# Optimization experiments

Measured on AMD Instinct MI355X. Metric: run time of the kernel, lower is better.

## Reference

```python
import jax, jax.numpy as jnp
import numpy as np

R, MAXI, MAXO = 333, 119, 12   # n ROIs, max roi input size, max roi reduced size
E, H = 3328, 8                  # embed dim (concat 3325 + pad 3), heads
HD = E // H                     # 416
CONCAT = 3325
EPS = 1e-5


def _roi_layout():
    """Deterministic synthetic ROI sizes + gather maps for vectorized ragged encode."""
    sizes = 30 + (7 * np.arange(R)) % 90            # per-ROI input widths
    reduced = 8 + np.arange(R) % 5                  # per-ROI output widths
    reduced[332] = 8                                # makes concat+3 divisible by 8
    starts = np.concatenate([[0], np.cumsum(sizes)[:-1]])
    total = int(sizes.sum())                        # 24696
    in_idx = np.minimum(starts[:, None] + np.arange(MAXI)[None, :], total - 1)
    in_mask = (np.arange(MAXI)[None, :] < sizes[:, None]).astype(np.float32)
    out_idx = np.concatenate([i * MAXO + np.arange(reduced[i]) for i in range(R)])
    assert out_idx.shape[0] == CONCAT
    return jnp.asarray(in_idx), jnp.asarray(in_mask), jnp.asarray(out_idx)


def _bn(x, g, b):
    # training-mode BatchNorm1d: biased batch stats (matches torch normalization)
    m = x.mean(0)
    v = x.var(0)
    return (x - m) * jax.lax.rsqrt(v + EPS) * g + b


def _lrelu(x, s):
    return jnp.where(x > 0, x, s * x)


def setup_inputs() -> dict:
    key = jax.random.key(0)
    ks = jax.random.split(key, 16)
    B, TOTAL = 2048, 24696
    f32 = jnp.float32
    return {
        'x': jax.random.normal(ks[0], (B, TOTAL), f32),
        'enc_W': jax.random.normal(ks[1], (R, MAXO, MAXI), f32) * 0.1,
        'enc_b': jax.random.normal(ks[2], (R, MAXO), f32) * 0.02,
        'bn1_g': jnp.ones((CONCAT,), f32),
        'bn1_b': jnp.zeros((CONCAT,), f32),
        'Wqkv': jax.random.normal(ks[3], (3 * E, E), f32) * (1.0 / np.sqrt(E)),
        'bqkv': jnp.zeros((3 * E,), f32),
        'Wo': jax.random.normal(ks[4], (E, E), f32) * (1.0 / np.sqrt(E)),
        'bo': jnp.zeros((E,), f32),
        'W1': jax.random.normal(ks[5], (1024, E), f32) * (1.0 / np.sqrt(E)),
        'b1': jnp.zeros((1024,), f32),
        'bn2_g': jnp.ones((1024,), f32),
        'bn2_b': jnp.zeros((1024,), f32),
        'W2': jax.random.normal(ks[6], (300, 1024), f32) * (1.0 / 32.0),
        'b2': jnp.zeros((300,), f32),
        'Wc': jax.random.normal(ks[7], (180, 300), f32) * 0.06,
        'bc': jnp.zeros((180,), f32),
    }


def reference(x, enc_W, enc_b, bn1_g, bn1_b, Wqkv, bqkv, Wo, bo,
              W1, b1, bn2_g, bn2_b, W2, b2, Wc, bc):
    in_idx, in_mask, out_idx = _roi_layout()
    B = x.shape[0]
    # --- vectorized ragged per-ROI Linear (replaces 333-way python loop) ---
    xp = x[:, in_idx] * in_mask                     # [B, R, MAXI], padded slices
    y = jnp.einsum('bri,roi->bro', xp, enc_W) + enc_b  # [B, R, MAXO]
    y = y.reshape(B, R * MAXO)[:, out_idx]          # ragged concat -> [B, 3325]
    # per-ROI BN+LeakyReLU(0.3) == per-feature on the concat
    y = _lrelu(_bn(y, bn1_g, bn1_b), 0.3)
    y = jnp.pad(y, ((0, 0), (1, 2)))                # F.pad (1, 2) -> [B, 3328]
    # --- MultiheadAttention, seq_len = 1 (input unsqueezed to [1, B, E]) ---
    qkv = y @ Wqkv.T + bqkv                         # [B, 3E]
    q, k, v = jnp.split(qkv, 3, axis=-1)
    q = q.reshape(B, H, 1, HD)
    k = k.reshape(B, H, 1, HD)
    v = v.reshape(B, H, 1, HD)
    s = jnp.einsum('bhqd,bhkd->bhqk', q, k) / jnp.sqrt(jnp.float32(HD))
    a = jax.nn.softmax(s, axis=-1)                  # trivially 1 for L=1, kept faithful
    o = jnp.einsum('bhqk,bhkd->bhqd', a, v).reshape(B, E)
    o = o @ Wo.T + bo
    r = _lrelu(_bn(o @ W1.T + b1, bn2_g, bn2_b), 0.1)
    reg_out = r @ W2.T + b2                         # [B, 300]
    y_pred = jax.nn.softmax(reg_out @ Wc.T + bc, axis=-1)  # [B, 180]
    return reg_out, y_pred
```

## Files before the change

### kernel.cpp

```cpp
#include <hip/hip_runtime.h>
#include <hip/hip_bf16.h>

#define B_      2048
#define R_      333
#define MAXI_   119
#define MAXO_   12
#define CONCAT_ 3325
#define E_      3328
#define TOTAL_  24696
#define HID_    1024
#define NREG_   300
#define NCLS_   180
#define EPS_    1e-5f
#define NS2_    128

typedef __attribute__((ext_vector_type(8))) short bf16x8;
typedef __attribute__((ext_vector_type(4))) float f32x4;

static __device__ inline unsigned short f2bf_rne(float f) {
  unsigned u;
  __builtin_memcpy(&u, &f, 4);
  u += 0x7fff + ((u >> 16) & 1);
  return (unsigned short)(u >> 16);
}
static __device__ inline float bf2f(unsigned short s) {
  unsigned u = (unsigned)s << 16;
  float f;
  __builtin_memcpy(&f, &u, 4);
  return f;
}

__global__ void layout_kernel(int* __restrict__ starts, int* __restrict__ red_starts) {
  if (threadIdx.x == 0 && blockIdx.x == 0) {
    int s = 0, rs = 0;
    for (int r = 0; r < R_; ++r) {
      starts[r] = s;
      red_starts[r] = rs;
      s += 30 + (7 * r) % 90;
      rs += (r == 332) ? 8 : (8 + r % 5);
    }
  }
}

__device__ __forceinline__ void rowdot_body(
    const float* __restrict__ A, const float* __restrict__ v, const float* __restrict__ b,
    float* __restrict__ out, int N, int K, int jb) {
  int wid = threadIdx.x >> 6, lane = threadIdx.x & 63;
  int j = jb * 4 + wid;
  if (j >= N) return;
  const float* row = A + (size_t)j * K;
  float s = 0.f;
  for (int k = lane; k < K; k += 64) s = fmaf(row[k], v[k], s);
  for (int o = 32; o; o >>= 1) s += __shfl_down(s, o);
  if (lane == 0) out[j] = s + b[j];
}

__device__ __forceinline__ void pack_w_body(const float* __restrict__ enc_W,
                                            const int* __restrict__ starts,
                                            unsigned short* __restrict__ Wpk, int r) {
  int tid = threadIdx.x;
  int kc = tid >> 6, lane = tid & 63;
  int size = 30 + (7 * r) % 90;
  int s8 = starts[r] & 7;
  int oc = lane & 15;
  int k0 = kc * 32 + (lane >> 4) * 8;
  unsigned short o[8];
#pragma unroll
  for (int e = 0; e < 8; ++e) {
    int k = k0 + e - s8;
    float v = 0.f;
    if (oc < MAXO_ && k >= 0 && k < size) v = enc_W[((size_t)r * MAXO_ + oc) * MAXI_ + k];
    o[e] = f2bf_rne(v);
  }
  unsigned short* dst = Wpk + ((size_t)r * 4 + kc) * 512 + lane * 8;
  *(ushort4*)dst = *(ushort4*)&o[0];
  *(ushort4*)(dst + 4) = *(ushort4*)&o[4];
}

#define NTR_    ((E_ / 64) * (E_ / 64))
#define NC4A_   (HID_ * E_ / 4)
#define NC4B_   (NREG_ * HID_ / 4)
#define NCAST_  ((NC4A_ + NC4B_ + 255) / 256)
__global__ __launch_bounds__(256) void prep_kernel(
    const float* __restrict__ Wo, const float* __restrict__ Wv,
    unsigned short* __restrict__ WoT, unsigned short* __restrict__ WvT,
    const float* __restrict__ W1, unsigned short* __restrict__ W1b,
    const float* __restrict__ W2, unsigned short* __restrict__ W2b,
    const float* __restrict__ bv, const float* __restrict__ bo, float* __restrict__ t1v,
    const float* __restrict__ enc_W, const int* __restrict__ starts,
    unsigned short* __restrict__ Wpk) {
  __shared__ float tile[64][65];
  int bid = blockIdx.x;
  if (bid < 2 * NTR_) {
    int z = bid / NTR_, rem = bid % NTR_;
    const float* in = z ? Wv : Wo;
    unsigned short* out = z ? WvT : WoT;
    int c0 = (rem % 52) * 64, r0 = (rem / 52) * 64;
    int t = threadIdx.x;
    int ci = t & 63, ri0 = t >> 6;
    for (int ri = ri0; ri < 64; ri += 4)
      tile[ri][ci] = in[(size_t)(r0 + ri) * E_ + c0 + ci];
    __syncthreads();
    int rj = t & 63, i0 = t >> 6;
    for (int i = i0; i < 64; i += 4)
      out[(size_t)(c0 + i) * E_ + r0 + rj] = f2bf_rne(tile[rj][i]);
  } else if (bid < 2 * NTR_ + NCAST_) {
    int i = (bid - 2 * NTR_) * 256 + threadIdx.x;
    const float* src; unsigned short* dst; int idx;
    if (i < NC4A_) { src = W1; dst = W1b; idx = i; }
    else if (i < NC4A_ + NC4B_) { src = W2; dst = W2b; idx = i - NC4A_; }
    else return;
    float4 v = ((const float4*)src)[idx];
    ushort4 o;
    o.x = f2bf_rne(v.x); o.y = f2bf_rne(v.y); o.z = f2bf_rne(v.z); o.w = f2bf_rne(v.w);
    ((ushort4*)dst)[idx] = o;
  } else if (bid < 2 * NTR_ + NCAST_ + E_ / 4) {
    rowdot_body(Wo, bv, bo, t1v, E_, E_, bid - 2 * NTR_ - NCAST_);
  } else {
    pack_w_body(enc_W, starts, Wpk, bid - 2 * NTR_ - NCAST_ - E_ / 4);
  }
}

__device__ __forceinline__ void encode_body(
    const float* __restrict__ x, const unsigned short* __restrict__ Wpk,
    const float* __restrict__ enc_b, const int* __restrict__ starts,
    const int* __restrict__ red_starts,
    unsigned short* __restrict__ yT, int r, int bg) {
  int tid = threadIdx.x;
  int wid = tid >> 6, lane = tid & 63;
  int lr = lane & 15, kg = lane >> 4;

  int size = 30 + (7 * r) % 90;
  int red  = (r == 332) ? 8 : (8 + r % 5);
  int st   = starts[r];
  int s8   = st & 7;
  int a0   = st & ~7;
  int rs   = red_starts[r];
  int nkc  = (s8 + size + 31) >> 5;
  int kmax = TOTAL_ - a0;

  bf16x8 wf[4];
  const unsigned short* wp = Wpk + (size_t)r * 2048 + lane * 8;
#pragma unroll
  for (int kc = 0; kc < 4; ++kc) wf[kc] = *(const bf16x8*)(wp + kc * 512);

  float bofs[4];
#pragma unroll
  for (int reg = 0; reg < 4; ++reg) {
    int oc = kg * 4 + reg;
    bofs[reg] = (oc < MAXO_) ? enc_b[r * MAXO_ + oc] : 0.f;
  }

  int b0 = bg * 64 + wid * 16;
  const float* xrow = x + (size_t)(b0 + lr) * TOTAL_ + a0;
  f32x4 acc = {0.f, 0.f, 0.f, 0.f};
#pragma unroll
  for (int kc = 0; kc < 4; ++kc) {
    if (kc < nkc) {
      int k0 = kc * 32 + kg * 8;
      if (k0 + 8 > kmax) k0 = kmax - 8;
      float4 v0 = *(const float4*)(xrow + k0);
      float4 v1 = *(const float4*)(xrow + k0 + 4);
      bf16x8 xf;
      xf[0] = (short)f2bf_rne(v0.x); xf[1] = (short)f2bf_rne(v0.y);
      xf[2] = (short)f2bf_rne(v0.z); xf[3] = (short)f2bf_rne(v0.w);
      xf[4] = (short)f2bf_rne(v1.x); xf[5] = (short)f2bf_rne(v1.y);
      xf[6] = (short)f2bf_rne(v1.z); xf[7] = (short)f2bf_rne(v1.w);
      acc = __builtin_amdgcn_mfma_f32_16x16x32_bf16(wf[kc], xf, acc, 0, 0, 0);
    }
  }
#pragma unroll
  for (int reg = 0; reg < 4; ++reg) {
    int oc = kg * 4 + reg;
    if (oc < red)
      yT[(size_t)(rs + oc) * B_ + b0 + lr] = f2bf_rne(acc[reg] + bofs[reg]);
  }
}

template <int KS, bool OUT_BF16>
__device__ __forceinline__ void gemm_body(
    const unsigned short* __restrict__ A, const unsigned short* __restrict__ W,
    float* __restrict__ Cf, unsigned short* __restrict__ Cb,
    int M, int N, int K, int bx, int by, int bz, unsigned short* smem) {
  unsigned short* a_lds = smem;
  unsigned short* b_lds = smem + 8192;
  int tid = threadIdx.x;
  int wid = tid >> 6, lane = tid & 63;
  int wr = wid >> 1, wc = wid & 1;
  int row0 = by * 128, col0 = bx * 128;
  int lr = lane & 15, kg = lane >> 4;
  int Klocal = K / KS;
  int kbase = bz * Klocal;

  int srow = tid >> 2, sk = (tid & 3) * 8;
  const unsigned short* aptr0 = A + (size_t)(row0 + srow) * K + kbase + sk;
  const unsigned short* aptr1 = aptr0 + (size_t)64 * K;
  int bcol0 = col0 + srow;      if (bcol0 > N - 1) bcol0 = N - 1;
  int bcol1 = col0 + 64 + srow; if (bcol1 > N - 1) bcol1 = N - 1;
  const unsigned short* bptr0 = W + (size_t)bcol0 * K + kbase + sk;
  const unsigned short* bptr1 = W + (size_t)bcol1 * K + kbase + sk;

  f32x4 acc[4][4] = {};
  int nk = Klocal >> 5;

#define STAGE_(buf, kc)                                                                             \
  do {                                                                                              \
    __builtin_amdgcn_global_load_lds((const __attribute__((address_space(1))) void*)(aptr0 + (kc)), \
        (__attribute__((address_space(3))) void*)(a_lds + (buf) * 4096 + wid * 512), 16, 0, 0);     \
    __builtin_amdgcn_global_load_lds((const __attribute__((address_space(1))) void*)(aptr1 + (kc)), \
        (__attribute__((address_space(3))) void*)(a_lds + (buf) * 4096 + 2048 + wid * 512), 16, 0, 0); \
    __builtin_amdgcn_global_load_lds((const __attribute__((address_space(1))) void*)(bptr0 + (kc)), \
        (__attribute__((address_space(3))) void*)(b_lds + (buf) * 4096 + wid * 512), 16, 0, 0);     \
    __builtin_amdgcn_global_load_lds((const __attribute__((address_space(1))) void*)(bptr1 + (kc)), \
        (__attribute__((address_space(3))) void*)(b_lds + (buf) * 4096 + 2048 + wid * 512), 16, 0, 0); \
  } while (0)

  STAGE_(0, 0);
  __syncthreads();
  int cur = 0;
  for (int t = 0; t < nk; ++t) {
    if (t + 1 < nk) STAGE_(cur ^ 1, (t + 1) * 32);
    bf16x8 a[4], b[4];
#pragma unroll
    for (int f = 0; f < 4; ++f) {
      a[f] = *(const bf16x8*)(a_lds + cur * 4096 + (wr * 64 + f * 16 + lr) * 32 + kg * 8);
      b[f] = *(const bf16x8*)(b_lds + cur * 4096 + (wc * 64 + f * 16 + lr) * 32 + kg * 8);
    }
#pragma unroll
    for (int i = 0; i < 4; ++i)
#pragma unroll
      for (int j = 0; j < 4; ++j)
        acc[i][j] = __builtin_amdgcn_mfma_f32_16x16x32_bf16(a[i], b[j], acc[i][j], 0, 0, 0);
    __syncthreads();
    cur ^= 1;
  }
#undef STAGE_

#pragma unroll
  for (int j = 0; j < 4; ++j) {
    int ccol = col0 + wc * 64 + j * 16 + lr;
    if (ccol >= N) continue;
#pragma unroll
    for (int i = 0; i < 4; ++i) {
#pragma unroll
      for (int reg = 0; reg < 4; ++reg) {
        int crow = row0 + wr * 64 + i * 16 + kg * 4 + reg;
        float v = acc[i][j][reg];
        if (KS == 1) {
          if (OUT_BF16) Cb[(size_t)crow * N + ccol] = f2bf_rne(v);
          else          Cf[(size_t)crow * N + ccol] = v;
        } else {
          Cf[((size_t)bz * M + crow) * N + ccol] = v;
        }
      }
    }
  }
}

#define WA_NB_   ((E_ / 128) * (HID_ / 128))
#define ENCH_NB_ (R_ * 16)
__global__ __launch_bounds__(256) void mega_a_kernel(
    const float* __restrict__ x, const unsigned short* __restrict__ Wpk,
    const float* __restrict__ enc_b, const int* __restrict__ starts,
    const int* __restrict__ red_starts, unsigned short* __restrict__ yT,
    const unsigned short* __restrict__ W1b, const unsigned short* __restrict__ WoT,
    unsigned short* __restrict__ Wa_bf,
    const float* __restrict__ W1, const float* __restrict__ t1v,
    const float* __restrict__ b1, float* __restrict__ zbv) {
  __shared__ __align__(16) unsigned short smem[16384];
  int bid = blockIdx.x;
  if (bid < WA_NB_) {
    gemm_body<1, true>(W1b, WoT, nullptr, Wa_bf, HID_, E_, E_,
                       bid % (E_ / 128), bid / (E_ / 128), 0, smem);
  } else if (bid < WA_NB_ + ENCH_NB_) {
    int eb = bid - WA_NB_;
    encode_body(x, Wpk, enc_b, starts, red_starts, yT, eb >> 4, eb & 15);
  } else {
    rowdot_body(W1, t1v, b1, zbv, HID_, E_, bid - WA_NB_ - ENCH_NB_);
  }
}

#define WB2_NB_ (WA_NB_ * 2)
__global__ __launch_bounds__(256) void mega_b_kernel(
    const float* __restrict__ x, const unsigned short* __restrict__ Wpk,
    const float* __restrict__ enc_b, const int* __restrict__ starts,
    const int* __restrict__ red_starts, unsigned short* __restrict__ yT,
    const unsigned short* __restrict__ Wa_bf, const unsigned short* __restrict__ WvT,
    float* __restrict__ Cpart) {
  __shared__ __align__(16) unsigned short smem[16384];
  int bid = blockIdx.x;
  if (bid < WB2_NB_) {
    int z = bid / WA_NB_, rem = bid % WA_NB_;
    gemm_body<2, false>(Wa_bf, WvT, Cpart, nullptr, HID_, E_, E_,
                        rem % (E_ / 128), rem / (E_ / 128), z, smem);
  } else {
    int eb = bid - WB2_NB_;
    encode_body(x, Wpk, enc_b, starts, red_starts, yT, eb >> 4, 16 + (eb & 15));
  }
}

#define ST_NB_  ((CONCAT_ + 15) / 16)
#define CWB_NB_ (HID_ * E_ / 4 / 256)
__global__ __launch_bounds__(256) void stats_comb_kernel(
    const unsigned short* __restrict__ yT, float* __restrict__ mean, float* __restrict__ rstd,
    const float* __restrict__ Cpart, unsigned short* __restrict__ Wb_bf) {
  int bid = blockIdx.x;
  if (bid < ST_NB_) {
    int t = threadIdx.x;
    int f = bid * 16 + (t >> 4);
    int j = t & 15;
    if (f >= CONCAT_) return;
    const unsigned short* p = yT + (size_t)f * B_ + j * 128;
    float s = 0.f, s2 = 0.f;
#pragma unroll
    for (int i = 0; i < 16; ++i) {
      bf16x8 v = *(const bf16x8*)(p + i * 8);
#pragma unroll
      for (int e = 0; e < 8; ++e) {
        float xv = bf2f((unsigned short)v[e]);
        s += xv; s2 = fmaf(xv, xv, s2);
      }
    }
#pragma unroll
    for (int m = 1; m <= 8; m <<= 1) { s += __shfl_xor(s, m); s2 += __shfl_xor(s2, m); }
    if (j == 0) {
      float mm = s / B_;
      float var = s2 / B_ - mm * mm;
      mean[f] = mm;
      rstd[f] = rsqrtf(var + EPS_);
    }
  } else {
    int i4 = (bid - ST_NB_) * 256 + threadIdx.x;
    const int MN4 = HID_ * E_ / 4;
    if (i4 >= MN4) return;
    float4 a = ((const float4*)Cpart)[i4];
    float4 b = ((const float4*)(Cpart + (size_t)HID_ * E_))[i4];
    ushort4 o;
    o.x = f2bf_rne(a.x + b.x); o.y = f2bf_rne(a.y + b.y);
    o.z = f2bf_rne(a.z + b.z); o.w = f2bf_rne(a.w + b.w);
    ((ushort4*)Wb_bf)[i4] = o;
  }
}

#define TR_NB_ ((E_ / 64) * (B_ / 64))
__global__ __launch_bounds__(256) void bn1_transpose_kernel(
    const unsigned short* __restrict__ yT, const float* __restrict__ mean,
    const float* __restrict__ rstd, const float* __restrict__ g,
    const float* __restrict__ bb, unsigned short* __restrict__ Y) {
  __shared__ float tile[64][65];
  int bid = blockIdx.x;
  int cc0 = (bid % 52) * 64, b0 = (bid / 52) * 64;
  int t = threadIdx.x;
  int bi = t & 63, ci0 = t >> 6;
  for (int ci = ci0; ci < 64; ci += 4) {
    int c = cc0 + ci - 1;
    float v = 0.f;
    if (c >= 0 && c < CONCAT_) {
      float f = bf2f(yT[(size_t)c * B_ + b0 + bi]);
      v = (f - mean[c]) * rstd[c] * g[c] + bb[c];
      v = v > 0.f ? v : 0.3f * v;
    }
    tile[ci][bi] = v;
  }
  __syncthreads();
  int cj = t & 63, bj0 = t >> 6;
  for (int bj = bj0; bj < 64; bj += 4)
    Y[(size_t)(b0 + bj) * E_ + cc0 + cj] = f2bf_rne(tile[cj][bj]);
}

template <int KS, bool OUT_BF16>
__global__ __launch_bounds__(256) void gemm_kernel(
    const unsigned short* __restrict__ A, const unsigned short* __restrict__ W,
    float* __restrict__ Cf, unsigned short* __restrict__ Cb, int M, int N, int K) {
  __shared__ __align__(16) unsigned short smem[16384];
  gemm_body<KS, OUT_BF16>(A, W, Cf, Cb, M, N, K, blockIdx.x, blockIdx.y, blockIdx.z, smem);
}

__global__ __launch_bounds__(256) void combZ_stats_kernel(
    const float* __restrict__ Cpart, const float* __restrict__ zb,
    float* __restrict__ Z, float* __restrict__ pS, float* __restrict__ pS2) {
  int c = blockIdx.x * 256 + threadIdx.x;
  int ry = blockIdx.y;
  float zbc = zb[c];
  float s1 = 0.f, s2 = 0.f;
  for (int r = ry * 16; r < ry * 16 + 16; ++r) {
    float v = zbc;
#pragma unroll
    for (int z = 0; z < 4; ++z) v += Cpart[((size_t)z * B_ + r) * HID_ + c];
    Z[(size_t)r * HID_ + c] = v;
    s1 += v; s2 = fmaf(v, v, s2);
  }
  pS[ry * HID_ + c] = s1;
  pS2[ry * HID_ + c] = s2;
}

__global__ __launch_bounds__(256) void colstats_final_kernel(
    const float* __restrict__ pS, const float* __restrict__ pS2,
    float* __restrict__ mean, float* __restrict__ rstd) {
  int c = blockIdx.x * 256 + threadIdx.x;
  if (c >= HID_) return;
  float s = 0.f, s2 = 0.f;
  for (int i = 0; i < NS2_; ++i) { s += pS[i * HID_ + c]; s2 += pS2[i * HID_ + c]; }
  float m = s / B_;
  float v = s2 / B_ - m * m;
  mean[c] = m;
  rstd[c] = rsqrtf(v + EPS_);
}

__global__ __launch_bounds__(256) void bn2_apply_kernel(
    const float* __restrict__ Z, const float* __restrict__ mean, const float* __restrict__ rstd,
    const float* __restrict__ g, const float* __restrict__ bb, unsigned short* __restrict__ R) {
  int i = blockIdx.x * 256 + threadIdx.x;
  int c = i & (HID_ - 1);
  float v = (Z[i] - mean[c]) * rstd[c] * g[c] + bb[c];
  v = v > 0.f ? v : 0.1f * v;
  R[i] = f2bf_rne(v);
}

__global__ __launch_bounds__(256) void classifier_kernel(
    const float* __restrict__ Cpart, const float* __restrict__ b2,
    const float* __restrict__ Wc, const float* __restrict__ bc,
    float* __restrict__ reg_out, float* __restrict__ ypred) {
  int b = blockIdx.x;
  __shared__ __align__(16) float rrow[NREG_];
  __shared__ float sl[256];
  int tid = threadIdx.x;
  for (int i = tid; i < NREG_; i += 256) {
    float s = b2[i];
#pragma unroll
    for (int z = 0; z < 4; ++z) s += Cpart[((size_t)z * B_ + b) * NREG_ + i];
    rrow[i] = s;
    reg_out[(size_t)b * NREG_ + i] = s;
  }
  __syncthreads();
  float s = -1e30f;
  if (tid < NCLS_) {
    const float* w = Wc + (size_t)tid * NREG_;
    float acc = 0.f;
    for (int k = 0; k < NREG_; k += 4) {
      float4 wv = *(const float4*)(w + k);
      float4 rv = *(const float4*)(&rrow[k]);
      acc = fmaf(wv.x, rv.x, acc); acc = fmaf(wv.y, rv.y, acc);
      acc = fmaf(wv.z, rv.z, acc); acc = fmaf(wv.w, rv.w, acc);
    }
    s = acc + bc[tid];
  }
  sl[tid] = s;
  __syncthreads();
  for (int o = 128; o > 0; o >>= 1) {
    if (tid < o) sl[tid] = fmaxf(sl[tid], sl[tid + o]);
    __syncthreads();
  }
  float mx = sl[0];
  __syncthreads();
  float e = (tid < NCLS_) ? __expf(s - mx) : 0.f;
  sl[tid] = e;
  __syncthreads();
  for (int o = 128; o > 0; o >>= 1) {
    if (tid < o) sl[tid] += sl[tid + o];
    __syncthreads();
  }
  if (tid < NCLS_) ypred[(size_t)b * NCLS_ + tid] = e / sl[0];
}

extern "C" void kernel_launch(void* const* d_in, const int* in_sizes, int n_in,
                              void* d_out, int out_size, void* d_ws, size_t ws_size,
                              hipStream_t stream) {
  const float* x     = (const float*)d_in[0];
  const float* enc_W = (const float*)d_in[1];
  const float* enc_b = (const float*)d_in[2];
  const float* bn1_g = (const float*)d_in[3];
  const float* bn1_b = (const float*)d_in[4];
  const float* Wqkv  = (const float*)d_in[5];
  const float* bqkv  = (const float*)d_in[6];
  const float* Wo    = (const float*)d_in[7];
  const float* bo    = (const float*)d_in[8];
  const float* W1    = (const float*)d_in[9];
  const float* b1    = (const float*)d_in[10];
  const float* bn2_g = (const float*)d_in[11];
  const float* bn2_b = (const float*)d_in[12];
  const float* W2    = (const float*)d_in[13];
  const float* b2    = (const float*)d_in[14];
  const float* Wc    = (const float*)d_in[15];
  const float* bc    = (const float*)d_in[16];

  char* ws = (char*)d_ws;
  size_t off = 0;
  auto alloc = [&](size_t bytes) -> void* {
    void* p = ws + off;
    off += (bytes + 255) & ~(size_t)255;
    return p;
  };

  unsigned short* yT     = (unsigned short*)alloc((size_t)CONCAT_ * B_ * 2);
  float*          mean1  = (float*)alloc(CONCAT_ * 4);
  float*          rstd1  = (float*)alloc(CONCAT_ * 4);
  unsigned short* Ybf    = (unsigned short*)alloc((size_t)B_ * E_ * 2);
  unsigned short* Rbf    = (unsigned short*)alloc((size_t)B_ * HID_ * 2);
  unsigned short* WoT_bf = (unsigned short*)alloc((size_t)E_ * E_ * 2);
  unsigned short* WvT_bf = (unsigned short*)alloc((size_t)E_ * E_ * 2);
  unsigned short* W1_bf  = (unsigned short*)alloc((size_t)HID_ * E_ * 2);
  unsigned short* W2_bf  = (unsigned short*)alloc((size_t)NREG_ * HID_ * 2);
  unsigned short* Wa_bf  = (unsigned short*)alloc((size_t)HID_ * E_ * 2);
  unsigned short* Wb_bf  = (unsigned short*)alloc((size_t)HID_ * E_ * 2);
  unsigned short* Wpk    = (unsigned short*)alloc((size_t)R_ * 2048 * 2);
  float*          Cpart  = (float*)alloc((size_t)4 * B_ * HID_ * 4);
  float*          t1v    = (float*)alloc(E_ * 4);
  float*          zbv    = (float*)alloc(HID_ * 4);
  float*          partS  = (float*)alloc((size_t)NS2_ * HID_ * 4);
  float*          partS2 = (float*)alloc((size_t)NS2_ * HID_ * 4);
  float*          mean2  = (float*)alloc(HID_ * 4);
  float*          rstd2  = (float*)alloc(HID_ * 4);
  int*            starts = (int*)alloc(R_ * 4);
  int*            redst  = (int*)alloc(R_ * 4);

  float* Z = (float*)yT;

  layout_kernel<<<1, 1, 0, stream>>>(starts, redst);
  prep_kernel<<<2 * NTR_ + NCAST_ + E_ / 4 + R_, 256, 0, stream>>>(
      Wo, Wqkv + (size_t)2 * E_ * E_, WoT_bf, WvT_bf,
      W1, W1_bf, W2, W2_bf, bqkv + 2 * E_, bo, t1v, enc_W, starts, Wpk);
  mega_a_kernel<<<WA_NB_ + ENCH_NB_ + HID_ / 4, 256, 0, stream>>>(
      x, Wpk, enc_b, starts, redst, yT, W1_bf, WoT_bf, Wa_bf, W1, t1v, b1, zbv);
  mega_b_kernel<<<WB2_NB_ + ENCH_NB_, 256, 0, stream>>>(
      x, Wpk, enc_b, starts, redst, yT, Wa_bf, WvT_bf, Cpart);
  stats_comb_kernel<<<ST_NB_ + CWB_NB_, 256, 0, stream>>>(
      yT, mean1, rstd1, Cpart, Wb_bf);
  bn1_transpose_kernel<<<TR_NB_, 256, 0, stream>>>(
      yT, mean1, rstd1, bn1_g, bn1_b, Ybf);
  gemm_kernel<4, false><<<dim3(HID_ / 128, B_ / 128, 4), 256, 0, stream>>>(
      Ybf, Wb_bf, Cpart, nullptr, B_, HID_, E_);
  combZ_stats_kernel<<<dim3(HID_ / 256, NS2_), 256, 0, stream>>>(Cpart, zbv, Z, partS, partS2);
  colstats_final_kernel<<<(HID_ + 255) / 256, 256, 0, stream>>>(partS, partS2, mean2, rstd2);
  bn2_apply_kernel<<<(B_ * HID_) / 256, 256, 0, stream>>>(Z, mean2, rstd2, bn2_g, bn2_b, Rbf);
  gemm_kernel<4, false><<<dim3((NREG_ + 127) / 128, B_ / 128, 4), 256, 0, stream>>>(
      Rbf, W2_bf, Cpart, nullptr, B_, NREG_, HID_);
  float* reg_out = (float*)d_out;
  classifier_kernel<<<B_, 256, 0, stream>>>(
      Cpart, b2, Wc, bc, reg_out, reg_out + (size_t)B_ * NREG_);
}
```

Baseline: 312.7 us.

## Stage x chunks in LDS for ROI encode; drop split-K in weight-fold GEMM

Result: slower. 360.3 us (+15.2%).

```diff
diff --git a/kernel.cpp b/kernel.cpp
--- a/kernel.cpp
+++ b/kernel.cpp
@@ -13,6 +13,9 @@
 #define NCLS_   180
 #define EPS_    1e-5f
 #define NS2_    128
+#define CHN_    49
+#define CHW_    640
+#define XSTR_   648
 
 typedef __attribute__((ext_vector_type(8))) short bf16x8;
 typedef __attribute__((ext_vector_type(4))) float f32x4;
@@ -30,12 +33,17 @@
   return f;
 }
 
-__global__ void layout_kernel(int* __restrict__ starts, int* __restrict__ red_starts) {
+__global__ void layout_kernel(int* __restrict__ starts, int* __restrict__ red_starts,
+                              int* __restrict__ chunk_first, int* __restrict__ chunk_cnt) {
   if (threadIdx.x == 0 && blockIdx.x == 0) {
+    for (int c = 0; c < CHN_; ++c) { chunk_first[c] = 0; chunk_cnt[c] = 0; }
     int s = 0, rs = 0;
     for (int r = 0; r < R_; ++r) {
       starts[r] = s;
       red_starts[r] = rs;
+      int c = s >> 9;
+      if (chunk_cnt[c] == 0) chunk_first[c] = r;
+      chunk_cnt[c]++;
       s += 30 + (7 * r) % 90;
       rs += (r == 332) ? 8 : (8 + r % 5);
     }
@@ -121,59 +129,58 @@
   }
 }
 
-__device__ __forceinline__ void encode_body(
+__device__ __forceinline__ void encode64_body(
     const float* __restrict__ x, const unsigned short* __restrict__ Wpk,
     const float* __restrict__ enc_b, const int* __restrict__ starts,
-    const int* __restrict__ red_starts,
-    unsigned short* __restrict__ yT, int r, int bg) {
+    const int* __restrict__ red_starts, const int* __restrict__ chunk_first,
+    const int* __restrict__ chunk_cnt, unsigned short* __restrict__ yT,
+    unsigned short* __restrict__ xt , int c, int bt) {
   int tid = threadIdx.x;
   int wid = tid >> 6, lane = tid & 63;
+  int base = c << 9;
+  int row0 = bt * 16;
+
+  for (int rr = wid * 4; rr < wid * 4 + 4; ++rr) {
+    const float* src = x + (size_t)(row0 + rr) * TOTAL_ + base;
+#pragma unroll
+    for (int j = 0; j < 3; ++j) {
+      int col = j * 256 + lane * 4;
+      if (col < CHW_) {
+        float4 v = {0.f, 0.f, 0.f, 0.f};
+        if (base + col < TOTAL_) v = *(const float4*)(src + col);
+        ushort4 o;
+        o.x = f2bf_rne(v.x); o.y = f2bf_rne(v.y); o.z = f2bf_rne(v.z); o.w = f2bf_rne(v.w);
+        *(ushort4*)&xt[rr * XSTR_ + col] = o;
+      }
+    }
+  }
+  __syncthreads();
+
   int lr = lane & 15, kg = lane >> 4;
-
-  int size = 30 + (7 * r) % 90;
-  int red  = (r == 332) ? 8 : (8 + r % 5);
-  int st   = starts[r];
-  int s8   = st & 7;
-  int a0   = st & ~7;
-  int rs   = red_starts[r];
-  int nkc  = (s8 + size + 31) >> 5;
-  int kmax = TOTAL_ - a0;
-
-  bf16x8 wf[4];
-  const unsigned short* wp = Wpk + (size_t)r * 2048 + lane * 8;
-#pragma unroll
-  for (int kc = 0; kc < 4; ++kc) wf[kc] = *(const bf16x8*)(wp + kc * 512);
-
-  float bofs[4];
-#pragma unroll
-  for (int reg = 0; reg < 4; ++reg) {
-    int oc = kg * 4 + reg;
-    bofs[reg] = (oc < MAXO_) ? enc_b[r * MAXO_ + oc] : 0.f;
-  }
-
-  int b0 = bg * 64 + wid * 16;
-  const float* xrow = x + (size_t)(b0 + lr) * TOTAL_ + a0;
-  f32x4 acc = {0.f, 0.f, 0.f, 0.f};
-#pragma unroll
-  for (int kc = 0; kc < 4; ++kc) {
-    if (kc < nkc) {
-      int k0 = kc * 32 + kg * 8;
-      if (k0 + 8 > kmax) k0 = kmax - 8;
-      float4 v0 = *(const float4*)(xrow + k0);
-      float4 v1 = *(const float4*)(xrow + k0 + 4);
-      bf16x8 xf;
-      xf[0] = (short)f2bf_rne(v0.x); xf[1] = (short)f2bf_rne(v0.y);
-      xf[2] = (short)f2bf_rne(v0.z); xf[3] = (short)f2bf_rne(v0.w);
-      xf[4] = (short)f2bf_rne(v1.x); xf[5] = (short)f2bf_rne(v1.y);
-      xf[6] = (short)f2bf_rne(v1.z); xf[7] = (short)f2bf_rne(v1.w);
-      acc = __builtin_amdgcn_mfma_f32_16x16x32_bf16(wf[kc], xf, acc, 0, 0, 0);
-    }
-  }
-#pragma unroll
-  for (int reg = 0; reg < 4; ++reg) {
-    int oc = kg * 4 + reg;
-    if (oc < red)
-      yT[(size_t)(rs + oc) * B_ + b0 + lr] = f2bf_rne(acc[reg] + bofs[reg]);
+  int first = chunk_first[c], cnt = chunk_cnt[c];
+  for (int ri = wid; ri < cnt; ri += 4) {
+    int r = first + ri;
+    int size = 30 + (7 * r) % 90;
+    int red  = (r == 332) ? 8 : (8 + r % 5);
+    int st   = starts[r];
+    int s8   = st & 7;
+    int ls8  = (st - base) & ~7;
+    int rs   = red_starts[r];
+    int nkc  = (s8 + size + 31) >> 5;
+
+    f32x4 acc = {0.f, 0.f, 0.f, 0.f};
+    const unsigned short* wp = Wpk + (size_t)r * 2048 + lane * 8;
+    for (int kc = 0; kc < nkc; ++kc) {
+      bf16x8 wf = *(const bf16x8*)(wp + kc * 512);
+      bf16x8 xf = *(const bf16x8*)&xt[lr * XSTR_ + ls8 + kc * 32 + kg * 8];
+      acc = __builtin_amdgcn_mfma_f32_16x16x32_bf16(wf, xf, acc, 0, 0, 0);
+    }
+#pragma unroll
+    for (int reg = 0; reg < 4; ++reg) {
+      int oc = kg * 4 + reg;
+      if (oc < red)
+        yT[(size_t)(rs + oc) * B_ + row0 + lr] = f2bf_rne(acc[reg] + enc_b[r * MAXO_ + oc]);
+    }
   }
 }
 
@@ -258,11 +265,12 @@
 }
 
 #define WA_NB_   ((E_ / 128) * (HID_ / 128))
-#define ENCH_NB_ (R_ * 16)
+#define ENCH_NB_ (CHN_ * 64)
 __global__ __launch_bounds__(256) void mega_a_kernel(
     const float* __restrict__ x, const unsigned short* __restrict__ Wpk,
     const float* __restrict__ enc_b, const int* __restrict__ starts,
-    const int* __restrict__ red_starts, unsigned short* __restrict__ yT,
+    const int* __restrict__ red_starts, const int* __restrict__ chF,
+    const int* __restrict__ chC, unsigned short* __restrict__ yT,
     const unsigned short* __restrict__ W1b, const unsigned short* __restrict__ WoT,
     unsigned short* __restrict__ Wa_bf,
     const float* __restrict__ W1, const float* __restrict__ t1v,
@@ -274,71 +282,57 @@
                        bid % (E_ / 128), bid / (E_ / 128), 0, smem);
   } else if (bid < WA_NB_ + ENCH_NB_) {
     int eb = bid - WA_NB_;
-    encode_body(x, Wpk, enc_b, starts, red_starts, yT, eb >> 4, eb & 15);
+    encode64_body(x, Wpk, enc_b, starts, red_starts, chF, chC, yT, smem,
+                  eb / 64, eb % 64);
   } else {
     rowdot_body(W1, t1v, b1, zbv, HID_, E_, bid - WA_NB_ - ENCH_NB_);
   }
 }
 
-#define WB2_NB_ (WA_NB_ * 2)
 __global__ __launch_bounds__(256) void mega_b_kernel(
     const float* __restrict__ x, const unsigned short* __restrict__ Wpk,
     const float* __restrict__ enc_b, const int* __restrict__ starts,
-    const int* __restrict__ red_starts, unsigned short* __restrict__ yT,
+    const int* __restrict__ red_starts, const int* __restrict__ chF,
+    const int* __restrict__ chC, unsigned short* __restrict__ yT,
     const unsigned short* __restrict__ Wa_bf, const unsigned short* __restrict__ WvT,
-    float* __restrict__ Cpart) {
+    unsigned short* __restrict__ Wb_bf) {
   __shared__ __align__(16) unsigned short smem[16384];
   int bid = blockIdx.x;
-  if (bid < WB2_NB_) {
-    int z = bid / WA_NB_, rem = bid % WA_NB_;
-    gemm_body<2, false>(Wa_bf, WvT, Cpart, nullptr, HID_, E_, E_,
-                        rem % (E_ / 128), rem / (E_ / 128), z, smem);
+  if (bid < WA_NB_) {
+    gemm_body<1, true>(Wa_bf, WvT, nullptr, Wb_bf, HID_, E_, E_,
+                       bid % (E_ / 128), bid / (E_ / 128), 0, smem);
   } else {
-    int eb = bid - WB2_NB_;
-    encode_body(x, Wpk, enc_b, starts, red_starts, yT, eb >> 4, 16 + (eb & 15));
+    int eb = bid - WA_NB_;
+    encode64_body(x, Wpk, enc_b, starts, red_starts, chF, chC, yT, smem,
+                  eb / 64, 64 + eb % 64);
   }
 }
 
 #define ST_NB_  ((CONCAT_ + 15) / 16)
-#define CWB_NB_ (HID_ * E_ / 4 / 256)
-__global__ __launch_bounds__(256) void stats_comb_kernel(
-    const unsigned short* __restrict__ yT, float* __restrict__ mean, float* __restrict__ rstd,
-    const float* __restrict__ Cpart, unsigned short* __restrict__ Wb_bf) {
-  int bid = blockIdx.x;
-  if (bid < ST_NB_) {
-    int t = threadIdx.x;
-    int f = bid * 16 + (t >> 4);
-    int j = t & 15;
-    if (f >= CONCAT_) return;
-    const unsigned short* p = yT + (size_t)f * B_ + j * 128;
-    float s = 0.f, s2 = 0.f;
-#pragma unroll
-    for (int i = 0; i < 16; ++i) {
-      bf16x8 v = *(const bf16x8*)(p + i * 8);
-#pragma unroll
-      for (int e = 0; e < 8; ++e) {
-        float xv = bf2f((unsigned short)v[e]);
-        s += xv; s2 = fmaf(xv, xv, s2);
-      }
-    }
-#pragma unroll
-    for (int m = 1; m <= 8; m <<= 1) { s += __shfl_xor(s, m); s2 += __shfl_xor(s2, m); }
-    if (j == 0) {
-      float mm = s / B_;
-      float var = s2 / B_ - mm * mm;
-      mean[f] = mm;
-      rstd[f] = rsqrtf(var + EPS_);
-    }
-  } else {
-    int i4 = (bid - ST_NB_) * 256 + threadIdx.x;
-    const int MN4 = HID_ * E_ / 4;
-    if (i4 >= MN4) return;
-    float4 a = ((const float4*)Cpart)[i4];
-    float4 b = ((const float4*)(Cpart + (size_t)HID_ * E_))[i4];
-    ushort4 o;
-    o.x = f2bf_rne(a.x + b.x); o.y = f2bf_rne(a.y + b.y);
-    o.z = f2bf_rne(a.z + b.z); o.w = f2bf_rne(a.w + b.w);
-    ((ushort4*)Wb_bf)[i4] = o;
+__global__ __launch_bounds__(256) void bn1_stats_kernel(
+    const unsigned short* __restrict__ yT, float* __restrict__ mean, float* __restrict__ rstd) {
+  int t = threadIdx.x;
+  int f = blockIdx.x * 16 + (t >> 4);
+  int j = t & 15;
+  if (f >= CONCAT_) return;
+  const unsigned short* p = yT + (size_t)f * B_ + j * 128;
+  float s = 0.f, s2 = 0.f;
+#pragma unroll
+  for (int i = 0; i < 16; ++i) {
+    bf16x8 v = *(const bf16x8*)(p + i * 8);
+#pragma unroll
+    for (int e = 0; e < 8; ++e) {
+      float xv = bf2f((unsigned short)v[e]);
+      s += xv; s2 = fmaf(xv, xv, s2);
+    }
+  }
+#pragma unroll
+  for (int m = 1; m <= 8; m <<= 1) { s += __shfl_xor(s, m); s2 += __shfl_xor(s2, m); }
+  if (j == 0) {
+    float mm = s / B_;
+    float var = s2 / B_ - mm * mm;
+    mean[f] = mm;
+    rstd[f] = rsqrtf(var + EPS_);
   }
 }
 
@@ -513,19 +507,20 @@
   float*          rstd2  = (float*)alloc(HID_ * 4);
   int*            starts = (int*)alloc(R_ * 4);
   int*            redst  = (int*)alloc(R_ * 4);
+  int*            chF    = (int*)alloc(CHN_ * 4);
+  int*            chC    = (int*)alloc(CHN_ * 4);
 
   float* Z = (float*)yT;
 
-  layout_kernel<<<1, 1, 0, stream>>>(starts, redst);
+  layout_kernel<<<1, 1, 0, stream>>>(starts, redst, chF, chC);
   prep_kernel<<<2 * NTR_ + NCAST_ + E_ / 4 + R_, 256, 0, stream>>>(
       Wo, Wqkv + (size_t)2 * E_ * E_, WoT_bf, WvT_bf,
       W1, W1_bf, W2, W2_bf, bqkv + 2 * E_, bo, t1v, enc_W, starts, Wpk);
   mega_a_kernel<<<WA_NB_ + ENCH_NB_ + HID_ / 4, 256, 0, stream>>>(
-      x, Wpk, enc_b, starts, redst, yT, W1_bf, WoT_bf, Wa_bf, W1, t1v, b1, zbv);
-  mega_b_kernel<<<WB2_NB_ + ENCH_NB_, 256, 0, stream>>>(
-      x, Wpk, enc_b, starts, redst, yT, Wa_bf, WvT_bf, Cpart);
-  stats_comb_kernel<<<ST_NB_ + CWB_NB_, 256, 0, stream>>>(
-      yT, mean1, rstd1, Cpart, Wb_bf);
+      x, Wpk, enc_b, starts, redst, chF, chC, yT, W1_bf, WoT_bf, Wa_bf, W1, t1v, b1, zbv);
+  mega_b_kernel<<<WA_NB_ + ENCH_NB_, 256, 0, stream>>>(
+      x, Wpk, enc_b, starts, redst, chF, chC, yT, Wa_bf, WvT_bf, Wb_bf);
+  bn1_stats_kernel<<<ST_NB_, 256, 0, stream>>>(yT, mean1, rstd1);
   bn1_transpose_kernel<<<TR_NB_, 256, 0, stream>>>(
       yT, mean1, rstd1, bn1_g, bn1_b, Ybf);
   gemm_kernel<4, false><<<dim3(HID_ / 128, B_ / 128, 4), 256, 0, stream>>>(
```

## Rebalance prep work across mega kernels and split BN1 stats into halves

Applied to the files above, without the earlier changes.

Measured after the change: 330.6 us. 1.06x slower.

```diff
diff --git a/kernel.cpp b/kernel.cpp
--- a/kernel.cpp
+++ b/kernel.cpp
@@ -77,47 +77,40 @@
   *(ushort4*)(dst + 4) = *(ushort4*)&o[4];
 }
 
-#define NTR_    ((E_ / 64) * (E_ / 64))
-#define NC4A_   (HID_ * E_ / 4)
-#define NC4B_   (NREG_ * HID_ / 4)
-#define NCAST_  ((NC4A_ + NC4B_ + 255) / 256)
+__device__ __forceinline__ void transpose_body(
+    const float* __restrict__ in, unsigned short* __restrict__ out,
+    int tileIdx, void* smem) {
+  float (*tile)[65] = (float(*)[65])smem;
+  int c0 = (tileIdx % 52) * 64, r0 = (tileIdx / 52) * 64;
+  int t = threadIdx.x;
+  int ci = t & 63, ri0 = t >> 6;
+  for (int ri = ri0; ri < 64; ri += 4)
+    tile[ri][ci] = in[(size_t)(r0 + ri) * E_ + c0 + ci];
+  __syncthreads();
+  int rj = t & 63, i0 = t >> 6;
+  for (int i = i0; i < 64; i += 4)
+    out[(size_t)(c0 + i) * E_ + r0 + rj] = f2bf_rne(tile[rj][i]);
+}
+
+#define NTR_     ((E_ / 64) * (E_ / 64))
+#define W1C_NB_  (HID_ * E_ / 4 / 256)
 __global__ __launch_bounds__(256) void prep_kernel(
-    const float* __restrict__ Wo, const float* __restrict__ Wv,
-    unsigned short* __restrict__ WoT, unsigned short* __restrict__ WvT,
+    const float* __restrict__ Wo, unsigned short* __restrict__ WoT,
     const float* __restrict__ W1, unsigned short* __restrict__ W1b,
-    const float* __restrict__ W2, unsigned short* __restrict__ W2b,
-    const float* __restrict__ bv, const float* __restrict__ bo, float* __restrict__ t1v,
     const float* __restrict__ enc_W, const int* __restrict__ starts,
     unsigned short* __restrict__ Wpk) {
   __shared__ float tile[64][65];
   int bid = blockIdx.x;
-  if (bid < 2 * NTR_) {
-    int z = bid / NTR_, rem = bid % NTR_;
-    const float* in = z ? Wv : Wo;
-    unsigned short* out = z ? WvT : WoT;
-    int c0 = (rem % 52) * 64, r0 = (rem / 52) * 64;
-    int t = threadIdx.x;
-    int ci = t & 63, ri0 = t >> 6;
-    for (int ri = ri0; ri < 64; ri += 4)
-      tile[ri][ci] = in[(size_t)(r0 + ri) * E_ + c0 + ci];
-    __syncthreads();
-    int rj = t & 63, i0 = t >> 6;
-    for (int i = i0; i < 64; i += 4)
-      out[(size_t)(c0 + i) * E_ + r0 + rj] = f2bf_rne(tile[rj][i]);
-  } else if (bid < 2 * NTR_ + NCAST_) {
-    int i = (bid - 2 * NTR_) * 256 + threadIdx.x;
-    const float* src; unsigned short* dst; int idx;
-    if (i < NC4A_) { src = W1; dst = W1b; idx = i; }
-    else if (i < NC4A_ + NC4B_) { src = W2; dst = W2b; idx = i - NC4A_; }
-    else return;
-    float4 v = ((const float4*)src)[idx];
+  if (bid < NTR_) {
+    transpose_body(Wo, WoT, bid, tile);
+  } else if (bid < NTR_ + W1C_NB_) {
+    int i = (bid - NTR_) * 256 + threadIdx.x;
+    float4 v = ((const float4*)W1)[i];
     ushort4 o;
     o.x = f2bf_rne(v.x); o.y = f2bf_rne(v.y); o.z = f2bf_rne(v.z); o.w = f2bf_rne(v.w);
-    ((ushort4*)dst)[idx] = o;
-  } else if (bid < 2 * NTR_ + NCAST_ + E_ / 4) {
-    rowdot_body(Wo, bv, bo, t1v, E_, E_, bid - 2 * NTR_ - NCAST_);
+    ((ushort4*)W1b)[i] = o;
   } else {
-    pack_w_body(enc_W, starts, Wpk, bid - 2 * NTR_ - NCAST_ - E_ / 4);
+    pack_w_body(enc_W, starts, Wpk, bid - NTR_ - W1C_NB_);
   }
 }
 
@@ -175,6 +168,29 @@
     if (oc < red)
       yT[(size_t)(rs + oc) * B_ + b0 + lr] = f2bf_rne(acc[reg] + bofs[reg]);
   }
+}
+
+__device__ __forceinline__ void stats_half_body(
+    const unsigned short* __restrict__ yT, float* __restrict__ pS1, float* __restrict__ pS2,
+    int fblk, int rowbase) {
+  int t = threadIdx.x;
+  int f = fblk * 16 + (t >> 4);
+  int j = t & 15;
+  if (f >= CONCAT_) return;
+  const unsigned short* p = yT + (size_t)f * B_ + rowbase + j * 64;
+  float s = 0.f, s2 = 0.f;
+#pragma unroll
+  for (int i = 0; i < 8; ++i) {
+    bf16x8 v = *(const bf16x8*)(p + i * 8);
+#pragma unroll
+    for (int e = 0; e < 8; ++e) {
+      float xv = bf2f((unsigned short)v[e]);
+      s += xv; s2 = fmaf(xv, xv, s2);
+    }
+  }
+#pragma unroll
+  for (int m = 1; m <= 8; m <<= 1) { s += __shfl_xor(s, m); s2 += __shfl_xor(s2, m); }
+  if (j == 0) { pS1[f] = s; pS2[f] = s2; }
 }
 
 template <int KS, bool OUT_BF16>
@@ -259,14 +275,18 @@
 
 #define WA_NB_   ((E_ / 128) * (HID_ / 128))
 #define ENCH_NB_ (R_ * 16)
+#define RD1_NB_  (E_ / 4)
+#define W2C_NB_  (NREG_ * HID_ / 4 / 256)
 __global__ __launch_bounds__(256) void mega_a_kernel(
     const float* __restrict__ x, const unsigned short* __restrict__ Wpk,
     const float* __restrict__ enc_b, const int* __restrict__ starts,
     const int* __restrict__ red_starts, unsigned short* __restrict__ yT,
     const unsigned short* __restrict__ W1b, const unsigned short* __restrict__ WoT,
     unsigned short* __restrict__ Wa_bf,
-    const float* __restrict__ W1, const float* __restrict__ t1v,
-    const float* __restrict__ b1, float* __restrict__ zbv) {
+    const float* __restrict__ Wv, unsigned short* __restrict__ WvT,
+    const float* __restrict__ Wo, const float* __restrict__ bv,
+    const float* __restrict__ bo, float* __restrict__ t1v,
+    const float* __restrict__ W2, unsigned short* __restrict__ W2b) {
   __shared__ __align__(16) unsigned short smem[16384];
   int bid = blockIdx.x;
   if (bid < WA_NB_) {
@@ -275,45 +295,64 @@
   } else if (bid < WA_NB_ + ENCH_NB_) {
     int eb = bid - WA_NB_;
     encode_body(x, Wpk, enc_b, starts, red_starts, yT, eb >> 4, eb & 15);
+  } else if (bid < WA_NB_ + ENCH_NB_ + NTR_) {
+    transpose_body(Wv, WvT, bid - WA_NB_ - ENCH_NB_, smem);
+  } else if (bid < WA_NB_ + ENCH_NB_ + NTR_ + RD1_NB_) {
+    rowdot_body(Wo, bv, bo, t1v, E_, E_, bid - WA_NB_ - ENCH_NB_ - NTR_);
   } else {
-    rowdot_body(W1, t1v, b1, zbv, HID_, E_, bid - WA_NB_ - ENCH_NB_);
+    int i = (bid - WA_NB_ - ENCH_NB_ - NTR_ - RD1_NB_) * 256 + threadIdx.x;
+    if (i < NREG_ * HID_ / 4) {
+      float4 v = ((const float4*)W2)[i];
+      ushort4 o;
+      o.x = f2bf_rne(v.x); o.y = f2bf_rne(v.y); o.z = f2bf_rne(v.z); o.w = f2bf_rne(v.w);
+      ((ushort4*)W2b)[i] = o;
+    }
   }
 }
 
 #define WB2_NB_ (WA_NB_ * 2)
+#define RD2_NB_ (HID_ / 4)
+#define STH_NB_ ((CONCAT_ + 15) / 16)
 __global__ __launch_bounds__(256) void mega_b_kernel(
     const float* __restrict__ x, const unsigned short* __restrict__ Wpk,
     const float* __restrict__ enc_b, const int* __restrict__ starts,
     const int* __restrict__ red_starts, unsigned short* __restrict__ yT,
     const unsigned short* __restrict__ Wa_bf, const unsigned short* __restrict__ WvT,
-    float* __restrict__ Cpart) {
+    float* __restrict__ Cpart,
+    const float* __restrict__ W1, const float* __restrict__ t1v,
+    const float* __restrict__ b1, float* __restrict__ zbv,
+    float* __restrict__ pS1h, float* __restrict__ pS2h) {
   __shared__ __align__(16) unsigned short smem[16384];
   int bid = blockIdx.x;
   if (bid < WB2_NB_) {
     int z = bid / WA_NB_, rem = bid % WA_NB_;
     gemm_body<2, false>(Wa_bf, WvT, Cpart, nullptr, HID_, E_, E_,
                         rem % (E_ / 128), rem / (E_ / 128), z, smem);
-  } else {
+  } else if (bid < WB2_NB_ + ENCH_NB_) {
     int eb = bid - WB2_NB_;
     encode_body(x, Wpk, enc_b, starts, red_starts, yT, eb >> 4, 16 + (eb & 15));
-  }
-}
-
-#define ST_NB_  ((CONCAT_ + 15) / 16)
+  } else if (bid < WB2_NB_ + ENCH_NB_ + RD2_NB_) {
+    rowdot_body(W1, t1v, b1, zbv, HID_, E_, bid - WB2_NB_ - ENCH_NB_);
+  } else {
+    stats_half_body(yT, pS1h, pS2h, bid - WB2_NB_ - ENCH_NB_ - RD2_NB_, 0);
+  }
+}
+
 #define CWB_NB_ (HID_ * E_ / 4 / 256)
 __global__ __launch_bounds__(256) void stats_comb_kernel(
-    const unsigned short* __restrict__ yT, float* __restrict__ mean, float* __restrict__ rstd,
+    const unsigned short* __restrict__ yT, const float* __restrict__ pS1h,
+    const float* __restrict__ pS2h, float* __restrict__ mean, float* __restrict__ rstd,
     const float* __restrict__ Cpart, unsigned short* __restrict__ Wb_bf) {
   int bid = blockIdx.x;
-  if (bid < ST_NB_) {
+  if (bid < STH_NB_) {
     int t = threadIdx.x;
     int f = bid * 16 + (t >> 4);
     int j = t & 15;
     if (f >= CONCAT_) return;
-    const unsigned short* p = yT + (size_t)f * B_ + j * 128;
+    const unsigned short* p = yT + (size_t)f * B_ + 1024 + j * 64;
     float s = 0.f, s2 = 0.f;
 #pragma unroll
-    for (int i = 0; i < 16; ++i) {
+    for (int i = 0; i < 8; ++i) {
       bf16x8 v = *(const bf16x8*)(p + i * 8);
 #pragma unroll
       for (int e = 0; e < 8; ++e) {
@@ -324,13 +363,14 @@
 #pragma unroll
     for (int m = 1; m <= 8; m <<= 1) { s += __shfl_xor(s, m); s2 += __shfl_xor(s2, m); }
     if (j == 0) {
+      s += pS1h[f]; s2 += pS2h[f];
       float mm = s / B_;
       float var = s2 / B_ - mm * mm;
       mean[f] = mm;
       rstd[f] = rsqrtf(var + EPS_);
     }
   } else {
-    int i4 = (bid - ST_NB_) * 256 + threadIdx.x;
+    int i4 = (bid - STH_NB_) * 256 + threadIdx.x;
     const int MN4 = HID_ * E_ / 4;
     if (i4 >= MN4) return;
     float4 a = ((const float4*)Cpart)[i4];
@@ -495,6 +535,8 @@
   unsigned short* yT     = (unsigned short*)alloc((size_t)CONCAT_ * B_ * 2);
   float*          mean1  = (float*)alloc(CONCAT_ * 4);
   float*          rstd1  = (float*)alloc(CONCAT_ * 4);
+  float*          pS1h   = (float*)alloc(CONCAT_ * 4);
+  float*          pS2h   = (float*)alloc(CONCAT_ * 4);
   unsigned short* Ybf    = (unsigned short*)alloc((size_t)B_ * E_ * 2);
   unsigned short* Rbf    = (unsigned short*)alloc((size_t)B_ * HID_ * 2);
   unsigned short* WoT_bf = (unsigned short*)alloc((size_t)E_ * E_ * 2);
@@ -517,15 +559,15 @@
   float* Z = (float*)yT;
 
   layout_kernel<<<1, 1, 0, stream>>>(starts, redst);
-  prep_kernel<<<2 * NTR_ + NCAST_ + E_ / 4 + R_, 256, 0, stream>>>(
-      Wo, Wqkv + (size_t)2 * E_ * E_, WoT_bf, WvT_bf,
-      W1, W1_bf, W2, W2_bf, bqkv + 2 * E_, bo, t1v, enc_W, starts, Wpk);
-  mega_a_kernel<<<WA_NB_ + ENCH_NB_ + HID_ / 4, 256, 0, stream>>>(
-      x, Wpk, enc_b, starts, redst, yT, W1_bf, WoT_bf, Wa_bf, W1, t1v, b1, zbv);
-  mega_b_kernel<<<WB2_NB_ + ENCH_NB_, 256, 0, stream>>>(
-      x, Wpk, enc_b, starts, redst, yT, Wa_bf, WvT_bf, Cpart);
-  stats_comb_kernel<<<ST_NB_ + CWB_NB_, 256, 0, stream>>>(
-      yT, mean1, rstd1, Cpart, Wb_bf);
+  prep_kernel<<<NTR_ + W1C_NB_ + R_, 256, 0, stream>>>(
+      Wo, WoT_bf, W1, W1_bf, enc_W, starts, Wpk);
+  mega_a_kernel<<<WA_NB_ + ENCH_NB_ + NTR_ + RD1_NB_ + W2C_NB_, 256, 0, stream>>>(
+      x, Wpk, enc_b, starts, redst, yT, W1_bf, WoT_bf, Wa_bf,
+      Wqkv + (size_t)2 * E_ * E_, WvT_bf, Wo, bqkv + 2 * E_, bo, t1v, W2, W2_bf);
+  mega_b_kernel<<<WB2_NB_ + ENCH_NB_ + RD2_NB_ + STH_NB_, 256, 0, stream>>>(
+      x, Wpk, enc_b, starts, redst, yT, Wa_bf, WvT_bf, Cpart, W1, t1v, b1, zbv, pS1h, pS2h);
+  stats_comb_kernel<<<STH_NB_ + CWB_NB_, 256, 0, stream>>>(
+      yT, pS1h, pS2h, mean1, rstd1, Cpart, Wb_bf);
   bn1_transpose_kernel<<<TR_NB_, 256, 0, stream>>>(
       yT, mean1, rstd1, bn1_g, bn1_b, Ybf);
   gemm_kernel<4, false><<<dim3(HID_ / 128, B_ / 128, 4), 256, 0, stream>>>(
```
